# Optimization experiments

Hardware: AMD Instinct MI355X
Metric: run time of the kernel (lower is better)

## Reference

```python
import math
import jax, jax.numpy as jnp
import numpy as np

B, N, G, D = 8, 1000, 1000, 2
E, H = 128, 8           # embedding_dim, n_heads
DH = E // H             # head dim
KNN = 16                # n_decoding_neighbors (static: mask all zeros -> K=min(16,N))
TANH_CLIP = 10.0


def make_heads(x, n_heads):
    # (B, n, E) -> (B, n_heads, n, E//n_heads)
    b, n, e = x.shape
    return x.reshape(b, n, n_heads, e // n_heads).transpose(0, 2, 1, 3)


def setup_inputs() -> dict:
    key = jax.random.key(0)
    ks = jax.random.split(key, 12)
    s = 1.0 / math.sqrt(E)
    return {
        "last_node": jax.random.randint(ks[0], (B, G), 0, N),
        "coordinates": jax.random.uniform(ks[1], (B, N, D), dtype=jnp.float32),
        "embeddings": jax.random.normal(ks[2], (B, N, E), dtype=jnp.float32),
        "group_ninf_mask": jnp.zeros((B, G, N), dtype=jnp.float32),
        "Wq_graph": jax.random.normal(ks[3], (E, E), dtype=jnp.float32) * s,
        "Wq_first": jax.random.normal(ks[4], (E, E), dtype=jnp.float32) * s,
        "Wq_last": jax.random.normal(ks[5], (E, E), dtype=jnp.float32) * s,
        "Wk": jax.random.normal(ks[6], (E, E), dtype=jnp.float32) * s,
        "Wv": jax.random.normal(ks[7], (E, E), dtype=jnp.float32) * s,
        "W_comb": jax.random.normal(ks[8], (E, E), dtype=jnp.float32) * s,
        "b_comb": jax.random.normal(ks[9], (E,), dtype=jnp.float32) * s,
    }


def reference(last_node, coordinates, embeddings, group_ninf_mask,
              Wq_graph, Wq_first, Wq_last, Wk, Wv, W_comb, b_comb):
    # --- reset() precomputation ---
    graph_emb = embeddings.mean(axis=1, keepdims=True)          # (B,1,E)
    q_graph = make_heads(graph_emb @ Wq_graph.T, H)             # (B,H,1,DH)
    k_h = make_heads(embeddings @ Wk.T, H)                      # (B,H,N,DH)
    v_h = make_heads(embeddings @ Wv.T, H)                      # (B,H,N,DH)

    # --- gather last node embedding ---
    idx_e = jnp.broadcast_to(last_node[..., None], (B, G, E))
    last_emb = jnp.take_along_axis(embeddings, idx_e, axis=1)   # (B,G,E)
    q_first = make_heads(last_emb @ Wq_first.T, H)              # (B,H,G,DH)
    q_last = make_heads(last_emb @ Wq_last.T, H)
    glimpse_q = q_graph + q_first + q_last                      # (B,H,G,DH)

    # --- KNN neighbor mask (cdist + topk + scatter) ---
    idx_c = jnp.broadcast_to(last_node[..., None], (B, G, D))
    last_coord = jnp.take_along_axis(coordinates, idx_c, axis=1)  # (B,G,D)
    d2 = (jnp.sum(last_coord**2, -1)[:, :, None]
          + jnp.sum(coordinates**2, -1)[:, None, :]
          - 2.0 * jnp.einsum('bgd,bnd->bgn', last_coord, coordinates))
    dist = jnp.sqrt(jnp.maximum(d2, 0.0))                       # (B,G,N)
    dist = jnp.where(group_ninf_mask == -jnp.inf, jnp.inf, dist)
    _, knn_idx = jax.lax.top_k(-dist, KNN)                      # (B,G,K) smallest dists
    bi = jnp.arange(B)[:, None, None]
    gi = jnp.arange(G)[None, :, None]
    glimpse_mask = jnp.full((B, G, N), -jnp.inf, dtype=jnp.float32)
    glimpse_mask = glimpse_mask.at[bi, gi, knn_idx].set(0.0)

    # --- masked multi-head glimpse attention ---
    scores = jnp.einsum('bhgd,bhnd->bhgn', glimpse_q, k_h) / math.sqrt(DH)
    scores = scores + glimpse_mask[:, None, :, :]
    attn = jax.nn.softmax(scores, axis=-1)
    out = jnp.einsum('bhgn,bhnd->bhgd', attn, v_h)              # (B,H,G,DH)
    out = out.transpose(0, 2, 1, 3).reshape(B, G, E)
    final_q = out @ W_comb.T + b_comb                           # (B,G,E)

    # --- tanh-clipped scoring + softmax ---
    score = jnp.einsum('bge,bne->bgn', final_q, embeddings) / math.sqrt(E)
    score_masked = TANH_CLIP * jnp.tanh(score) + group_ninf_mask
    probs = jax.nn.softmax(score_masked, axis=2)                # (B,G,N)
    return probs
```

## Files before the change

### kernel.cpp

```cpp
#include <hip/hip_runtime.h>
#include <math.h>

#define BD 8
#define NN 1000
#define GG 1000
#define EE 128

#define OFF_QG    0
#define OFF_K     1024
#define OFF_V     (OFF_K + 1024000)
#define OFF_QFL   (OFF_V + 1024000)
#define OFF_OUTG  (OFF_QFL + 1024000)
#define OFF_FQ    (OFF_OUTG + 1024000)
#define OFF_PART  (OFF_FQ + 1024000)

__global__ __launch_bounds__(1024) void k_graphq(const float* __restrict__ emb,
                                                 const float* __restrict__ Wqg,
                                                 float* __restrict__ qg) {
  __shared__ float partial[8][128];
  __shared__ float ge[128];
  int b = blockIdx.x;
  int t = threadIdx.x;
  int e = t & 127, p = t >> 7;
  const float* eb = emb + (size_t)b * NN * EE;
  float s = 0.f;
  int n0 = p * 125;
  for (int n = n0; n < n0 + 125; ++n) s += eb[(size_t)n * EE + e];
  partial[p][e] = s;
  __syncthreads();
  if (t < 128) {
    float m = 0.f;
#pragma unroll
    for (int q = 0; q < 8; ++q) m += partial[q][t];
    ge[t] = m * (1.f / 1000.f);
  }
  __syncthreads();
  if (t < 128) {
    const float* wr = Wqg + (size_t)t * EE;
    float acc = 0.f;
#pragma unroll 8
    for (int k = 0; k < 128; ++k) acc += ge[k] * wr[k];
    qg[b * EE + t] = acc;
  }
}

__global__ __launch_bounds__(256) void k_proj(const float* __restrict__ emb,
                                              const float* __restrict__ Wk,
                                              const float* __restrict__ Wv,
                                              const float* __restrict__ Wqf,
                                              const float* __restrict__ Wql,
                                              float* __restrict__ Karr,
                                              float* __restrict__ Varr,
                                              float* __restrict__ QFL) {
  __shared__ float Als[16][68];
  __shared__ float Bls[16][68];
  int mt = blockIdx.x, nt = blockIdx.y;
  int t = threadIdx.x;
  int ty = t >> 4, tx = t & 15;
  int row4 = t >> 2, kq = t & 3;
  float acc[4][4] = {};
  for (int k0 = 0; k0 < 128; k0 += 16) {
    const float* ap = emb + (size_t)(mt * 64 + row4) * EE + k0 + kq * 4;
    float4 av = *(const float4*)ap;
    int j = nt * 64 + row4;
    float4 bv;
    if (j < 128) {
      bv = *(const float4*)(Wk + (size_t)j * EE + k0 + kq * 4);
    } else if (j < 256) {
      bv = *(const float4*)(Wv + (size_t)(j - 128) * EE + k0 + kq * 4);
    } else {
      float4 f = *(const float4*)(Wqf + (size_t)(j - 256) * EE + k0 + kq * 4);
      float4 l = *(const float4*)(Wql + (size_t)(j - 256) * EE + k0 + kq * 4);
      bv = make_float4(f.x + l.x, f.y + l.y, f.z + l.z, f.w + l.w);
    }
    Als[kq * 4 + 0][row4] = av.x; Als[kq * 4 + 1][row4] = av.y;
    Als[kq * 4 + 2][row4] = av.z; Als[kq * 4 + 3][row4] = av.w;
    Bls[kq * 4 + 0][row4] = bv.x; Bls[kq * 4 + 1][row4] = bv.y;
    Bls[kq * 4 + 2][row4] = bv.z; Bls[kq * 4 + 3][row4] = bv.w;
    __syncthreads();
#pragma unroll
    for (int k = 0; k < 16; ++k) {
      float a0 = Als[k][ty * 4 + 0], a1 = Als[k][ty * 4 + 1];
      float a2 = Als[k][ty * 4 + 2], a3 = Als[k][ty * 4 + 3];
      float b0 = Bls[k][tx * 4 + 0], b1 = Bls[k][tx * 4 + 1];
      float b2 = Bls[k][tx * 4 + 2], b3 = Bls[k][tx * 4 + 3];
      acc[0][0] += a0 * b0; acc[0][1] += a0 * b1; acc[0][2] += a0 * b2; acc[0][3] += a0 * b3;
      acc[1][0] += a1 * b0; acc[1][1] += a1 * b1; acc[1][2] += a1 * b2; acc[1][3] += a1 * b3;
      acc[2][0] += a2 * b0; acc[2][1] += a2 * b1; acc[2][2] += a2 * b2; acc[2][3] += a2 * b3;
      acc[3][0] += a3 * b0; acc[3][1] += a3 * b1; acc[3][2] += a3 * b2; acc[3][3] += a3 * b3;
    }
    __syncthreads();
  }
  float* outp; int cb;
  if (nt < 2)      { outp = Karr; cb = nt * 64; }
  else if (nt < 4) { outp = Varr; cb = (nt - 2) * 64; }
  else             { outp = QFL;  cb = (nt - 4) * 64; }
#pragma unroll
  for (int i = 0; i < 4; ++i) {
    int r = mt * 64 + ty * 4 + i;
    float4 v = make_float4(acc[i][0], acc[i][1], acc[i][2], acc[i][3]);
    *(float4*)(outp + (size_t)r * EE + cb + tx * 4) = v;
  }
}

__global__ __launch_bounds__(256) void k_glimpse(const int* __restrict__ last_node,
                                                 const float* __restrict__ coords,
                                                 const float* __restrict__ mask,
                                                 const float* __restrict__ qg,
                                                 const float* __restrict__ QFL,
                                                 const float* __restrict__ Karr,
                                                 const float* __restrict__ Varr,
                                                 float* __restrict__ outg) {
  const float INF = __builtin_inff();
  int wid = (blockIdx.x * blockDim.x + threadIdx.x) >> 6;
  int lane = threadIdx.x & 63;
  int b = wid / GG, g = wid % GG;
  int last = last_node[b * GG + g];
  const float* cb = coords + (size_t)b * NN * 2;
  float lcx = cb[last * 2 + 0], lcy = cb[last * 2 + 1];
  float lc2 = lcx * lcx + lcy * lcy;
  const float* mrow = mask + ((size_t)b * GG + g) * NN;
  float d2v[16];
#pragma unroll
  for (int i = 0; i < 16; ++i) {
    int n = lane + 64 * i;
    float v = INF;
    if (n < NN) {
      float cx = cb[n * 2 + 0], cy = cb[n * 2 + 1];
      float d2 = lc2 + (cx * cx + cy * cy) - 2.f * (lcx * cx + lcy * cy);
      if (mrow[n] == -INF) d2 = INF;
      v = d2;
    }
    d2v[i] = v;
  }
  int h = lane >> 3;
  int kk = lane & 7;
  int n0sel = 0, n1sel = 0;
#pragma unroll
  for (int s = 0; s < 16; ++s) {
    float bestv = d2v[0]; int bestn = lane;
#pragma unroll
    for (int i = 1; i < 16; ++i) {
      int n = lane + 64 * i;
      float v = d2v[i];
      if (v < bestv) { bestv = v; bestn = n; }
    }
#pragma unroll
    for (int off = 1; off < 64; off <<= 1) {
      float ov = __shfl_xor(bestv, off);
      int on = __shfl_xor(bestn, off);
      if (ov < bestv || (ov == bestv && on < bestn)) { bestv = ov; bestn = on; }
    }
    if (s == kk) n0sel = bestn;
    if (s == kk + 8) n1sel = bestn;
#pragma unroll
    for (int i = 0; i < 16; ++i)
      if (lane + 64 * i == bestn) d2v[i] = INF;
  }
  float qh[16];
  const float* qfl = QFL + ((size_t)b * GG + last) * EE + h * 16;
  const float* qgb = qg + b * EE + h * 16;
#pragma unroll
  for (int d = 0; d < 16; ++d) qh[d] = qgb[d] + qfl[d];
  const float* Kb = Karr + (size_t)b * NN * EE;
  const float* k0p = Kb + (size_t)n0sel * EE + h * 16;
  const float* k1p = Kb + (size_t)n1sel * EE + h * 16;
  float s0 = 0.f, s1 = 0.f;
#pragma unroll
  for (int d = 0; d < 16; ++d) { s0 += qh[d] * k0p[d]; s1 += qh[d] * k1p[d]; }
  s0 *= 0.25f; s1 *= 0.25f;
  float m = fmaxf(s0, s1);
#pragma unroll
  for (int off = 1; off < 8; off <<= 1) m = fmaxf(m, __shfl_xor(m, off));
  float e0 = expf(s0 - m), e1 = expf(s1 - m);
  float se = e0 + e1;
#pragma unroll
  for (int off = 1; off < 8; off <<= 1) se += __shfl_xor(se, off);
  float p0 = e0 / se, p1 = e1 / se;
  const float* Vb = Varr + (size_t)b * NN * EE;
  float o0 = 0.f, o1 = 0.f;
#pragma unroll
  for (int k = 0; k < 16; ++k) {
    int src = h * 8 + (k & 7);
    float pk = (k < 8) ? __shfl(p0, src) : __shfl(p1, src);
    int nk = (k < 8) ? __shfl(n0sel, src) : __shfl(n1sel, src);
    const float* vp = Vb + (size_t)nk * EE + h * 16 + kk * 2;
    o0 += pk * vp[0]; o1 += pk * vp[1];
  }
  float* op = outg + ((size_t)b * GG + g) * EE + lane * 2;
  op[0] = o0; op[1] = o1;
}

__global__ __launch_bounds__(256) void k_comb(const float* __restrict__ outg,
                                              const float* __restrict__ Wc,
                                              const float* __restrict__ bc,
                                              float* __restrict__ fq) {
  __shared__ float Als[16][68];
  __shared__ float Bls[16][68];
  int mt = blockIdx.x, nt = blockIdx.y;
  int t = threadIdx.x;
  int ty = t >> 4, tx = t & 15;
  int row4 = t >> 2, kq = t & 3;
  float acc[4][4] = {};
  for (int k0 = 0; k0 < 128; k0 += 16) {
    float4 av = *(const float4*)(outg + (size_t)(mt * 64 + row4) * EE + k0 + kq * 4);
    int j = nt * 64 + row4;
    float4 bv = *(const float4*)(Wc + (size_t)j * EE + k0 + kq * 4);
    Als[kq * 4 + 0][row4] = av.x; Als[kq * 4 + 1][row4] = av.y;
    Als[kq * 4 + 2][row4] = av.z; Als[kq * 4 + 3][row4] = av.w;
    Bls[kq * 4 + 0][row4] = bv.x; Bls[kq * 4 + 1][row4] = bv.y;
    Bls[kq * 4 + 2][row4] = bv.z; Bls[kq * 4 + 3][row4] = bv.w;
    __syncthreads();
#pragma unroll
    for (int k = 0; k < 16; ++k) {
      float a0 = Als[k][ty * 4 + 0], a1 = Als[k][ty * 4 + 1];
      float a2 = Als[k][ty * 4 + 2], a3 = Als[k][ty * 4 + 3];
      float b0 = Bls[k][tx * 4 + 0], b1 = Bls[k][tx * 4 + 1];
      float b2 = Bls[k][tx * 4 + 2], b3 = Bls[k][tx * 4 + 3];
      acc[0][0] += a0 * b0; acc[0][1] += a0 * b1; acc[0][2] += a0 * b2; acc[0][3] += a0 * b3;
      acc[1][0] += a1 * b0; acc[1][1] += a1 * b1; acc[1][2] += a1 * b2; acc[1][3] += a1 * b3;
      acc[2][0] += a2 * b0; acc[2][1] += a2 * b1; acc[2][2] += a2 * b2; acc[2][3] += a2 * b3;
      acc[3][0] += a3 * b0; acc[3][1] += a3 * b1; acc[3][2] += a3 * b2; acc[3][3] += a3 * b3;
    }
    __syncthreads();
  }
#pragma unroll
  for (int i = 0; i < 4; ++i) {
    int r = mt * 64 + ty * 4 + i;
    int c = nt * 64 + tx * 4;
    float4 v = make_float4(acc[i][0] + bc[c + 0], acc[i][1] + bc[c + 1],
                           acc[i][2] + bc[c + 2], acc[i][3] + bc[c + 3]);
    *(float4*)(fq + (size_t)r * EE + c) = v;
  }
}

__global__ __launch_bounds__(256) void k_score(const float* __restrict__ fq,
                                               const float* __restrict__ emb,
                                               const float* __restrict__ mask,
                                               float* __restrict__ out,
                                               float* __restrict__ part) {
  __shared__ float Als[16][68];
  __shared__ float Bls[16][68];
  int b = blockIdx.x, gt = blockIdx.y, nt = blockIdx.z;
  int t = threadIdx.x;
  int ty = t >> 4, tx = t & 15;
  int row4 = t >> 2, kq = t & 3;
  int g0 = gt * 64, n0 = nt * 64;
  const float* A = fq + (size_t)b * GG * EE;
  const float* Bm = emb + (size_t)b * NN * EE;
  float acc[4][4] = {};
  for (int k0 = 0; k0 < 128; k0 += 16) {
    int gr = g0 + row4, nr = n0 + row4;
    float4 av = make_float4(0.f, 0.f, 0.f, 0.f), bv = av;
    if (gr < GG) av = *(const float4*)(A + (size_t)gr * EE + k0 + kq * 4);
    if (nr < NN) bv = *(const float4*)(Bm + (size_t)nr * EE + k0 + kq * 4);
    Als[kq * 4 + 0][row4] = av.x; Als[kq * 4 + 1][row4] = av.y;
    Als[kq * 4 + 2][row4] = av.z; Als[kq * 4 + 3][row4] = av.w;
    Bls[kq * 4 + 0][row4] = bv.x; Bls[kq * 4 + 1][row4] = bv.y;
    Bls[kq * 4 + 2][row4] = bv.z; Bls[kq * 4 + 3][row4] = bv.w;
    __syncthreads();
#pragma unroll
    for (int k = 0; k < 16; ++k) {
      float a0 = Als[k][ty * 4 + 0], a1 = Als[k][ty * 4 + 1];
      float a2 = Als[k][ty * 4 + 2], a3 = Als[k][ty * 4 + 3];
      float b0 = Bls[k][tx * 4 + 0], b1 = Bls[k][tx * 4 + 1];
      float b2 = Bls[k][tx * 4 + 2], b3 = Bls[k][tx * 4 + 3];
      acc[0][0] += a0 * b0; acc[0][1] += a0 * b1; acc[0][2] += a0 * b2; acc[0][3] += a0 * b3;
      acc[1][0] += a1 * b0; acc[1][1] += a1 * b1; acc[1][2] += a1 * b2; acc[1][3] += a1 * b3;
      acc[2][0] += a2 * b0; acc[2][1] += a2 * b1; acc[2][2] += a2 * b2; acc[2][3] += a2 * b3;
      acc[3][0] += a3 * b0; acc[3][1] += a3 * b1; acc[3][2] += a3 * b2; acc[3][3] += a3 * b3;
    }
    __syncthreads();
  }
  const float rs = 0.08838834764831845f;
#pragma unroll
  for (int i = 0; i < 4; ++i) {
    int g = g0 + ty * 4 + i;
    bool gv = (g < GG);
    const float* mrow = mask + ((size_t)b * GG + g) * NN;
    float* orow = out + ((size_t)b * GG + g) * NN;
    float rsacc = 0.f;
#pragma unroll
    for (int j = 0; j < 4; ++j) {
      int n = n0 + tx * 4 + j;
      float e = 0.f;
      if (gv && n < NN) {
        float sc = acc[i][j] * rs;
        float sm = 10.f * tanhf(sc) + mrow[n];
        e = expf(sm);
        orow[n] = e;
      }
      rsacc += e;
    }
#pragma unroll
    for (int off = 1; off < 16; off <<= 1) rsacc += __shfl_xor(rsacc, off);
    if (tx == 0 && gv) part[((size_t)b * GG + g) * 16 + nt] = rsacc;
  }
}

__global__ __launch_bounds__(256) void k_norm(const float* __restrict__ part,
                                              float* __restrict__ out) {
  int row = blockIdx.x;
  __shared__ float ssum;
  int t = threadIdx.x;
  float v = (t < 16) ? part[(size_t)row * 16 + t] : 0.f;
#pragma unroll
  for (int off = 1; off < 16; off <<= 1) v += __shfl_xor(v, off);
  if (t == 0) ssum = v;
  __syncthreads();
  float inv = 1.f / ssum;
  if (t < 250) {
    float4* o = (float4*)(out + (size_t)row * NN);
    float4 x = o[t];
    x.x *= inv; x.y *= inv; x.z *= inv; x.w *= inv;
    o[t] = x;
  }
}

extern "C" void kernel_launch(void* const* d_in, const int* in_sizes, int n_in,
                              void* d_out, int out_size, void* d_ws, size_t ws_size,
                              hipStream_t stream) {
  const int*   last_node = (const int*)d_in[0];
  const float* coords    = (const float*)d_in[1];
  const float* emb       = (const float*)d_in[2];
  const float* mask      = (const float*)d_in[3];
  const float* Wqg       = (const float*)d_in[4];
  const float* Wqf       = (const float*)d_in[5];
  const float* Wql       = (const float*)d_in[6];
  const float* Wk        = (const float*)d_in[7];
  const float* Wv        = (const float*)d_in[8];
  const float* Wc        = (const float*)d_in[9];
  const float* bc        = (const float*)d_in[10];
  float* out = (float*)d_out;
  float* ws  = (float*)d_ws;

  float* qg   = ws + OFF_QG;
  float* Karr = ws + OFF_K;
  float* Varr = ws + OFF_V;
  float* QFL  = ws + OFF_QFL;
  float* outg = ws + OFF_OUTG;
  float* fq   = ws + OFF_FQ;
  float* part = ws + OFF_PART;

  k_graphq<<<dim3(BD), dim3(1024), 0, stream>>>(emb, Wqg, qg);
  k_proj<<<dim3(125, 6), dim3(256), 0, stream>>>(emb, Wk, Wv, Wqf, Wql, Karr, Varr, QFL);
  k_glimpse<<<dim3(2000), dim3(256), 0, stream>>>(last_node, coords, mask, qg, QFL, Karr, Varr, outg);
  k_comb<<<dim3(125, 2), dim3(256), 0, stream>>>(outg, Wc, bc, fq);
  k_score<<<dim3(8, 16, 16), dim3(256), 0, stream>>>(fq, emb, mask, out, part);
  k_norm<<<dim3(8000), dim3(256), 0, stream>>>(part, out);
}
```

Measured before the change: 236.3 us.

## Enlarge score GEMM tile to 128x128 with register prefetch and fast tanh

Rewrites the score kernel to use 128x128 tiles with an 8x8 per-thread micro-tile, vectorised LDS reads and register prefetching of the next K-slice. This raises arithmetic intensity and overlaps global loads with compute. The epilogue now uses vectorised mask loads and output stores, and computes tanh through fast exp and reciprocal intrinsics. It also clamps the squared distance to be non-negative. The fast tanh may lose some accuracy, and 128 accumulators per thread raise register pressure.

```diff
diff --git a/kernel.cpp b/kernel.cpp
--- a/kernel.cpp
+++ b/kernel.cpp
@@ -128,6 +128,7 @@
     if (n < NN) {
       float cx = cb[n * 2 + 0], cy = cb[n * 2 + 1];
       float d2 = lc2 + (cx * cx + cy * cy) - 2.f * (lcx * cx + lcy * cy);
+      d2 = fmaxf(d2, 0.f);
       if (mrow[n] == -INF) d2 = INF;
       v = d2;
     }
@@ -234,67 +235,108 @@
   }
 }
 
-__global__ __launch_bounds__(256) void k_score(const float* __restrict__ fq,
-                                               const float* __restrict__ emb,
-                                               const float* __restrict__ mask,
-                                               float* __restrict__ out,
-                                               float* __restrict__ part) {
-  __shared__ float Als[16][68];
-  __shared__ float Bls[16][68];
+__global__ __launch_bounds__(256, 2) void k_score(const float* __restrict__ fq,
+                                                  const float* __restrict__ emb,
+                                                  const float* __restrict__ mask,
+                                                  float* __restrict__ out,
+                                                  float* __restrict__ part) {
+  __shared__ float As[16][132];
+  __shared__ float Bs[16][132];
   int b = blockIdx.x, gt = blockIdx.y, nt = blockIdx.z;
   int t = threadIdx.x;
-  int ty = t >> 4, tx = t & 15;
-  int row4 = t >> 2, kq = t & 3;
-  int g0 = gt * 64, n0 = nt * 64;
+  int tx = t & 15, ty = t >> 4;
+  int g0 = gt * 128, n0 = nt * 128;
   const float* A = fq + (size_t)b * GG * EE;
   const float* Bm = emb + (size_t)b * NN * EE;
-  float acc[4][4] = {};
+  int lr = t >> 1;
+  int lq = t & 1;
+  int ar = min(g0 + lr, GG - 1);
+  int br = min(n0 + lr, NN - 1);
+  const float* apos = A + (size_t)ar * EE + lq * 8;
+  const float* bpos = Bm + (size_t)br * EE + lq * 8;
+
+  float acc[8][8] = {};
+  float4 sa0 = *(const float4*)(apos + 0);
+  float4 sa1 = *(const float4*)(apos + 4);
+  float4 sb0 = *(const float4*)(bpos + 0);
+  float4 sb1 = *(const float4*)(bpos + 4);
   for (int k0 = 0; k0 < 128; k0 += 16) {
-    int gr = g0 + row4, nr = n0 + row4;
-    float4 av = make_float4(0.f, 0.f, 0.f, 0.f), bv = av;
-    if (gr < GG) av = *(const float4*)(A + (size_t)gr * EE + k0 + kq * 4);
-    if (nr < NN) bv = *(const float4*)(Bm + (size_t)nr * EE + k0 + kq * 4);
-    Als[kq * 4 + 0][row4] = av.x; Als[kq * 4 + 1][row4] = av.y;
-    Als[kq * 4 + 2][row4] = av.z; Als[kq * 4 + 3][row4] = av.w;
-    Bls[kq * 4 + 0][row4] = bv.x; Bls[kq * 4 + 1][row4] = bv.y;
-    Bls[kq * 4 + 2][row4] = bv.z; Bls[kq * 4 + 3][row4] = bv.w;
-    __syncthreads();
+    __syncthreads();
+    As[lq * 8 + 0][lr] = sa0.x; As[lq * 8 + 1][lr] = sa0.y;
+    As[lq * 8 + 2][lr] = sa0.z; As[lq * 8 + 3][lr] = sa0.w;
+    As[lq * 8 + 4][lr] = sa1.x; As[lq * 8 + 5][lr] = sa1.y;
+    As[lq * 8 + 6][lr] = sa1.z; As[lq * 8 + 7][lr] = sa1.w;
+    Bs[lq * 8 + 0][lr] = sb0.x; Bs[lq * 8 + 1][lr] = sb0.y;
+    Bs[lq * 8 + 2][lr] = sb0.z; Bs[lq * 8 + 3][lr] = sb0.w;
+    Bs[lq * 8 + 4][lr] = sb1.x; Bs[lq * 8 + 5][lr] = sb1.y;
+    Bs[lq * 8 + 6][lr] = sb1.z; Bs[lq * 8 + 7][lr] = sb1.w;
+    __syncthreads();
+    if (k0 < 112) {
+      sa0 = *(const float4*)(apos + k0 + 16);
+      sa1 = *(const float4*)(apos + k0 + 20);
+      sb0 = *(const float4*)(bpos + k0 + 16);
+      sb1 = *(const float4*)(bpos + k0 + 20);
+    }
 #pragma unroll
     for (int k = 0; k < 16; ++k) {
-      float a0 = Als[k][ty * 4 + 0], a1 = Als[k][ty * 4 + 1];
-      float a2 = Als[k][ty * 4 + 2], a3 = Als[k][ty * 4 + 3];
-      float b0 = Bls[k][tx * 4 + 0], b1 = Bls[k][tx * 4 + 1];
-      float b2 = Bls[k][tx * 4 + 2], b3 = Bls[k][tx * 4 + 3];
-      acc[0][0] += a0 * b0; acc[0][1] += a0 * b1; acc[0][2] += a0 * b2; acc[0][3] += a0 * b3;
-      acc[1][0] += a1 * b0; acc[1][1] += a1 * b1; acc[1][2] += a1 * b2; acc[1][3] += a1 * b3;
-      acc[2][0] += a2 * b0; acc[2][1] += a2 * b1; acc[2][2] += a2 * b2; acc[2][3] += a2 * b3;
-      acc[3][0] += a3 * b0; acc[3][1] += a3 * b1; acc[3][2] += a3 * b2; acc[3][3] += a3 * b3;
-    }
-    __syncthreads();
-  }
+      float4 av0 = *(const float4*)&As[k][ty * 8];
+      float4 av1 = *(const float4*)&As[k][ty * 8 + 4];
+      float4 bv0 = *(const float4*)&Bs[k][tx * 8];
+      float4 bv1 = *(const float4*)&Bs[k][tx * 8 + 4];
+      float af[8] = {av0.x, av0.y, av0.z, av0.w, av1.x, av1.y, av1.z, av1.w};
+      float bf[8] = {bv0.x, bv0.y, bv0.z, bv0.w, bv1.x, bv1.y, bv1.z, bv1.w};
+#pragma unroll
+      for (int i = 0; i < 8; ++i)
+#pragma unroll
+        for (int j = 0; j < 8; ++j) acc[i][j] += af[i] * bf[j];
+    }
+  }
+
   const float rs = 0.08838834764831845f;
-#pragma unroll
-  for (int i = 0; i < 4; ++i) {
-    int g = g0 + ty * 4 + i;
-    bool gv = (g < GG);
-    const float* mrow = mask + ((size_t)b * GG + g) * NN;
-    float* orow = out + ((size_t)b * GG + g) * NN;
-    float rsacc = 0.f;
-#pragma unroll
-    for (int j = 0; j < 4; ++j) {
-      int n = n0 + tx * 4 + j;
-      float e = 0.f;
-      if (gv && n < NN) {
-        float sc = acc[i][j] * rs;
-        float sm = 10.f * tanhf(sc) + mrow[n];
-        e = expf(sm);
-        orow[n] = e;
+  const float NEGINF = -__builtin_inff();
+  int gbase = g0 + ty * 8;
+  int nb = n0 + tx * 8;
+  bool nfull = (nb + 7 < NN);
+#pragma unroll
+  for (int i = 0; i < 8; ++i) {
+    int g = gbase + i;
+    int gc = g < GG ? g : GG - 1;
+    const float* mrow = mask + ((size_t)b * GG + gc) * NN;
+    float* orow = out + ((size_t)b * GG + gc) * NN;
+    float mv[8];
+    if (nfull) {
+      float4 m0 = *(const float4*)(mrow + nb);
+      float4 m1 = *(const float4*)(mrow + nb + 4);
+      mv[0] = m0.x; mv[1] = m0.y; mv[2] = m0.z; mv[3] = m0.w;
+      mv[4] = m1.x; mv[5] = m1.y; mv[6] = m1.z; mv[7] = m1.w;
+    } else {
+#pragma unroll
+      for (int j = 0; j < 8; ++j) mv[j] = (nb + j < NN) ? mrow[nb + j] : NEGINF;
+    }
+    float e[8];
+    float rsum = 0.f;
+#pragma unroll
+    for (int j = 0; j < 8; ++j) {
+      float sc = acc[i][j] * rs;
+      float u = __expf(2.f * sc);
+      float th = 1.f - 2.f * __builtin_amdgcn_rcpf(u + 1.f);
+      float ev = __expf(10.f * th + mv[j]);
+      e[j] = ev;
+      rsum += ev;
+    }
+    if (g < GG) {
+      if (nfull) {
+        *(float4*)(orow + nb)     = make_float4(e[0], e[1], e[2], e[3]);
+        *(float4*)(orow + nb + 4) = make_float4(e[4], e[5], e[6], e[7]);
+      } else {
+#pragma unroll
+        for (int j = 0; j < 8; ++j)
+          if (nb + j < NN) orow[nb + j] = e[j];
       }
-      rsacc += e;
-    }
-#pragma unroll
-    for (int off = 1; off < 16; off <<= 1) rsacc += __shfl_xor(rsacc, off);
-    if (tx == 0 && gv) part[((size_t)b * GG + g) * 16 + nt] = rsacc;
+    }
+#pragma unroll
+    for (int off = 1; off < 16; off <<= 1) rsum += __shfl_xor(rsum, off);
+    if (tx == 0 && g < GG) part[((size_t)b * GG + g) * 8 + nt] = rsum;
   }
 }
 
@@ -303,9 +345,9 @@
   int row = blockIdx.x;
   __shared__ float ssum;
   int t = threadIdx.x;
-  float v = (t < 16) ? part[(size_t)row * 16 + t] : 0.f;
-#pragma unroll
-  for (int off = 1; off < 16; off <<= 1) v += __shfl_xor(v, off);
+  float v = (t < 8) ? part[(size_t)row * 8 + t] : 0.f;
+#pragma unroll
+  for (int off = 1; off < 8; off <<= 1) v += __shfl_xor(v, off);
   if (t == 0) ssum = v;
   __syncthreads();
   float inv = 1.f / ssum;
@@ -346,6 +388,6 @@
   k_proj<<<dim3(125, 6), dim3(256), 0, stream>>>(emb, Wk, Wv, Wqf, Wql, Karr, Varr, QFL);
   k_glimpse<<<dim3(2000), dim3(256), 0, stream>>>(last_node, coords, mask, qg, QFL, Karr, Varr, outg);
   k_comb<<<dim3(125, 2), dim3(256), 0, stream>>>(outg, Wc, bc, fq);
-  k_score<<<dim3(8, 16, 16), dim3(256), 0, stream>>>(fq, emb, mask, out, part);
+  k_score<<<dim3(8, 8, 8), dim3(256), 0, stream>>>(fq, emb, mask, out, part);
   k_norm<<<dim3(8000), dim3(256), 0, stream>>>(part, out);
 }
```

Result: faster. 227.9 us (-3.6%).
